# Kernel tuning notes

Measured on AMD Instinct MI355X. Metric: run time of the kernel, lower is better.

Reference implementation:

```python
import jax, jax.numpy as jnp
import numpy as np
from jax import lax

WINDOW_SIZE = 11
SIGMA = 1.5
C1 = 0.01 ** 2
C2 = 0.03 ** 2


def _gaussian_window(channel, window_size=WINDOW_SIZE, sigma=SIGMA, dtype=jnp.float32):
    x = jnp.arange(window_size, dtype=dtype) - window_size // 2
    g = jnp.exp(-(x ** 2) / (2.0 * sigma ** 2))
    g = g / g.sum()
    w2 = jnp.outer(g, g)  # [K, K]
    # depthwise kernel: [C_out=C, C_in/groups=1, K, K]
    return jnp.broadcast_to(w2[None, None], (channel, 1, window_size, window_size))


def _dwconv(x, window, channel, window_size=WINDOW_SIZE):
    pad = window_size // 2
    return lax.conv_general_dilated(
        x, window,
        window_strides=(1, 1),
        padding=[(pad, pad), (pad, pad)],
        dimension_numbers=('NCHW', 'OIHW', 'NCHW'),
        feature_group_count=channel,
    )


def setup_inputs() -> dict:
    key = jax.random.key(0)
    k1, k2 = jax.random.split(key)
    img1 = jax.random.uniform(k1, (16, 3, 512, 512), dtype=jnp.float32)
    img2 = jax.random.uniform(k2, (16, 3, 512, 512), dtype=jnp.float32)
    return {"img1": img1, "img2": img2}


def reference(img1, img2):
    channel = img1.shape[1]
    window = _gaussian_window(channel, dtype=img1.dtype)

    mu1 = _dwconv(img1, window, channel)
    mu2 = _dwconv(img2, window, channel)
    mu1_sq = mu1 * mu1
    mu2_sq = mu2 * mu2
    mu1_mu2 = mu1 * mu2

    sigma1_sq = _dwconv(img1 * img1, window, channel) - mu1_sq
    sigma2_sq = _dwconv(img2 * img2, window, channel) - mu2_sq
    sigma12 = _dwconv(img1 * img2, window, channel) - mu1_mu2

    ssim_map = ((2.0 * mu1_mu2 + C1) * (2.0 * sigma12 + C2)) / (
        (mu1_sq + mu2_sq + C1) * (sigma1_sq + sigma2_sq + C2))
    return ssim_map.mean()
```

## Files before the change

### kernel.cpp

```cpp
#include <hip/hip_runtime.h>

namespace {
constexpr int IMG_W = 512, IMG_H = 512;
constexpr int TW = 32, TH = 32;
constexpr int IN_H = TH + 10;
constexpr float C1c = 0.01f * 0.01f;
constexpr float C2c = 0.03f * 0.03f;

constexpr float GW[11] = {
    1.0283799e-03f, 7.5987582e-03f, 3.6000773e-02f, 1.0936069e-01f,
    2.1300554e-01f, 2.6601172e-01f, 2.1300554e-01f, 1.0936069e-01f,
    3.6000773e-02f, 7.5987582e-03f, 1.0283799e-03f
};

using v2f = __attribute__((ext_vector_type(2))) float;
using v4f = __attribute__((ext_vector_type(4))) float;

__device__ __forceinline__ void pkfma(v2f& acc, v2f w, v2f a) {
    asm("v_pk_fma_f32 %0, %1, %2, %0" : "+v"(acc) : "s"(w), "v"(a));
}
__device__ __forceinline__ v2f pkfma3(v2f a, v2f b, v2f c) {
    v2f d;
    asm("v_pk_fma_f32 %0, %1, %2, %3" : "=v"(d) : "v"(a), "v"(b), "v"(c));
    return d;
}
__device__ __forceinline__ v2f pkmul(v2f a, v2f b) {
    v2f d;
    asm("v_pk_mul_f32 %0, %1, %2" : "=v"(d) : "v"(a), "v"(b));
    return d;
}
__device__ __forceinline__ v2f pkadd(v2f a, v2f b) {
    v2f d;
    asm("v_pk_add_f32 %0, %1, %2" : "=v"(d) : "v"(a), "v"(b));
    return d;
}
__device__ __forceinline__ v2f bcast(float w) { v2f r; r.x = w; r.y = w; return r; }

__device__ __forceinline__ int hswz(int row, int pc) {
    return row * 16 + ((pc + row) & 15);
}
}

__global__ __launch_bounds__(256, 6) void ssim_tile_kernel(
        const float* __restrict__ img1, const float* __restrict__ img2,
        double* __restrict__ acc)
{
    union SharedU {
        v4f raw[IN_H * 23];
        struct {
            v4f hA[IN_H * 16];
            v4f hB[IN_H * 16];
        } h;
    };
    __shared__ SharedU u;
    __shared__ float wred[4];

    const int tid = threadIdx.x;
    const size_t base = (size_t)blockIdx.z * (IMG_W * IMG_H);
    const float* p1 = img1 + base;
    const float* p2 = img2 + base;
    const int x0e = blockIdx.x * TW - 6;
    const int y0  = blockIdx.y * TH - 5;

    {
        v4f* s12v4 = u.raw;
        int r   = tid / 22;
        int cf2 = tid - r * 22;
        int goff = (y0 + r) * IMG_W + x0e + 2 * cf2;
        int soff = r * 23 + cf2;
        const bool interior =
            blockIdx.x > 0 && blockIdx.x < gridDim.x - 1 &&
            blockIdx.y > 0 && blockIdx.y < gridDim.y - 1;
        if (interior) {
#pragma unroll
            for (int i = 0; i < 4; ++i) {
                if (i < 3 || tid < 924 - 3 * 256) {
                    const float2 a = *(const float2*)&p1[goff];
                    const float2 b = *(const float2*)&p2[goff];
                    v4f q; q.x = a.x; q.y = b.x; q.z = a.y; q.w = b.y;
                    s12v4[soff] = q;
                }
                const bool wrap = cf2 + 14 >= 22;
                cf2  += wrap ? -8 : 14;
                r    += wrap ? 12 : 11;
                goff += wrap ? 12 * IMG_W - 16 : 11 * IMG_W + 28;
                soff += wrap ? 12 * 23 - 8     : 11 * 23 + 14;
            }
        } else {
#pragma unroll
            for (int i = 0; i < 4; ++i) {
                if (i < 3 || tid < 924 - 3 * 256) {
                    const int gy = y0 + r;
                    const int gx = x0e + 2 * cf2;
                    float a0 = 0.f, a1 = 0.f, b0 = 0.f, b1 = 0.f;
                    if (gy >= 0 && gy < IMG_H) {
                        if (gx >= 0 && gx < IMG_W)         { a0 = p1[goff];     b0 = p2[goff]; }
                        if (gx + 1 >= 0 && gx + 1 < IMG_W) { a1 = p1[goff + 1]; b1 = p2[goff + 1]; }
                    }
                    v4f q; q.x = a0; q.y = b0; q.z = a1; q.w = b1;
                    s12v4[soff] = q;
                }
                const bool wrap = cf2 + 14 >= 22;
                cf2  += wrap ? -8 : 14;
                r    += wrap ? 12 : 11;
                goff += wrap ? 12 * IMG_W - 16 : 11 * IMG_W + 28;
                soff += wrap ? 12 * 23 - 8     : 11 * 23 + 14;
            }
        }
    }
    __syncthreads();

    v2f mu8[8], sx8[8];
    const int rA = tid >> 2;
    const int gA = tid & 3;
    const bool act2 = tid < 168;
    if (act2) {
#pragma unroll
        for (int j = 0; j < 8; ++j) { mu8[j] = bcast(0.f); sx8[j] = bcast(0.f); }
        const v4f* srow = u.raw + (rA * 23 + gA * 4);
#pragma unroll
        for (int m = 0; m < 10; ++m) {
            const v4f q = srow[m];
            const v2f* qh = (const v2f*)&q;
#pragma unroll
            for (int half = 0; half < 2; ++half) {
                const int k = 2 * m + half;
                const v2f v = qh[half];
                const v2f a2 = pkmul(v, v);
                v2f sx;
                sx.x = a2.x + a2.y;
                sx.y = v.x * v.y;
#pragma unroll
                for (int j = 0; j < 8; ++j) {
                    const int t = k - j - 1;
                    if (t >= 0 && t < 11) {
                        const v2f w2 = bcast(GW[t]);
                        pkfma(mu8[j], w2, v);
                        pkfma(sx8[j], w2, sx);
                    }
                }
            }
        }
    }
    __syncthreads();
    if (act2) {
#pragma unroll
        for (int jp = 0; jp < 4; ++jp) {
            const int j0 = 2 * jp, j1 = 2 * jp + 1;
            v4f A; A.x = mu8[j0].x; A.y = mu8[j1].x; A.z = mu8[j0].y; A.w = mu8[j1].y;
            v4f B; B.x = sx8[j0].x; B.y = sx8[j1].x; B.z = sx8[j0].y; B.w = sx8[j1].y;
            const int e = hswz(rA, 4 * gA + jp);
            u.h.hA[e] = A;
            u.h.hB[e] = B;
        }
    }
    __syncthreads();

    float lsum = 0.f;
    if (tid < 128) {
        const int pc = tid & 15;
        const int rb = (tid >> 4) * 4;
        v2f m1[4], m2[4], ssA[4], xyA[4];
#pragma unroll
        for (int j = 0; j < 4; ++j) {
            m1[j] = bcast(0.f); m2[j] = bcast(0.f);
            ssA[j] = bcast(0.f); xyA[j] = bcast(0.f);
        }
#pragma unroll
        for (int k = 0; k < 14; ++k) {
            const int e = hswz(rb + k, pc);
            const v4f A = u.h.hA[e];
            const v4f B = u.h.hB[e];
            const v2f* ah = (const v2f*)&A;
            const v2f* bh = (const v2f*)&B;
#pragma unroll
            for (int j = 0; j < 4; ++j) {
                const int t = k - j;
                if (t >= 0 && t < 11) {
                    const v2f w2 = bcast(GW[t]);
                    pkfma(m1[j],  w2, ah[0]);
                    pkfma(m2[j],  w2, ah[1]);
                    pkfma(ssA[j], w2, bh[0]);
                    pkfma(xyA[j], w2, bh[1]);
                }
            }
        }
        const v2f two  = bcast(2.f);
        const v2f c1p  = bcast(C1c);
        const v2f c2p  = bcast(C2c);
        const v2f neg1 = bcast(-1.f);
#pragma unroll
        for (int j = 0; j < 4; ++j) {
            const v2f mu12 = pkmul(m1[j], m2[j]);
            const v2f sden = pkadd(pkmul(m1[j], m1[j]), pkmul(m2[j], m2[j]));
            const v2f s12  = pkfma3(mu12, neg1, xyA[j]);
            const v2f ssum = pkfma3(sden, neg1, ssA[j]);
            const v2f num  = pkmul(pkfma3(mu12, two, c1p), pkfma3(s12, two, c2p));
            const v2f den  = pkmul(pkadd(sden, c1p), pkadd(ssum, c2p));
            lsum += __fdividef(num.x, den.x) + __fdividef(num.y, den.y);
        }
    }

#pragma unroll
    for (int off = 32; off > 0; off >>= 1)
        lsum += __shfl_down(lsum, off, 64);
    if ((tid & 63) == 0) wred[tid >> 6] = lsum;
    __syncthreads();
    if (tid == 0) {
        const int bid = (blockIdx.z * gridDim.y + blockIdx.y) * gridDim.x + blockIdx.x;
        unsafeAtomicAdd(&acc[bid & 255],
                        (double)(wred[0] + wred[1] + wred[2] + wred[3]));
    }
}

__global__ __launch_bounds__(256) void ssim_final_kernel(
        const double* __restrict__ acc, float* __restrict__ out, double inv_total)
{
    const int tid = threadIdx.x;
    double a = acc[tid];
#pragma unroll
    for (int off = 32; off > 0; off >>= 1)
        a += __shfl_down(a, off, 64);
    __shared__ double ws[4];
    if ((tid & 63) == 0) ws[tid >> 6] = a;
    __syncthreads();
    if (tid == 0)
        out[0] = (float)((ws[0] + ws[1] + ws[2] + ws[3]) * inv_total);
}

extern "C" void kernel_launch(void* const* d_in, const int* in_sizes, int n_in,
                              void* d_out, int out_size, void* d_ws, size_t ws_size,
                              hipStream_t stream)
{
    const float* img1 = (const float*)d_in[0];
    const float* img2 = (const float*)d_in[1];
    double* acc = (double*)d_ws;

    hipMemsetAsync(d_ws, 0, 256 * sizeof(double), stream);

    const int nch = in_sizes[0] / (IMG_W * IMG_H);
    dim3 grid(IMG_W / TW, IMG_H / TH, nch);
    ssim_tile_kernel<<<grid, 256, 0, stream>>>(img1, img2, acc);

    const double inv_total = 1.0 / (double)in_sizes[0];
    ssim_final_kernel<<<1, 256, 0, stream>>>(acc, (float*)d_out, inv_total);
}
```

Baseline: 152.5 us.

## Load horizontal-pass inputs directly from global memory, skipping shared staging

The horizontal convolution threads now read their 20-wide row segments straight from global memory into registers instead of first staging the input tile in shared memory. This removes the cooperative staging store, one shared read pass and two barriers, and the union aliasing of shared buffers. In exchange, overlapping halo columns are fetched redundantly from global memory (served by cache), only 168 of 256 threads issue loads, and register pressure rises from the 40 staged floats per thread.

```diff
diff --git a/kernel.cpp b/kernel.cpp
--- a/kernel.cpp
+++ b/kernel.cpp
@@ -45,14 +45,8 @@
         const float* __restrict__ img1, const float* __restrict__ img2,
         double* __restrict__ acc)
 {
-    union SharedU {
-        v4f raw[IN_H * 23];
-        struct {
-            v4f hA[IN_H * 16];
-            v4f hB[IN_H * 16];
-        } h;
-    };
-    __shared__ SharedU u;
+    __shared__ v4f hA[IN_H * 16];
+    __shared__ v4f hB[IN_H * 16];
     __shared__ float wred[4];
 
     const int tid = threadIdx.x;
@@ -62,70 +56,53 @@
     const int x0e = blockIdx.x * TW - 6;
     const int y0  = blockIdx.y * TH - 5;
 
-    {
-        v4f* s12v4 = u.raw;
-        int r   = tid / 22;
-        int cf2 = tid - r * 22;
-        int goff = (y0 + r) * IMG_W + x0e + 2 * cf2;
-        int soff = r * 23 + cf2;
+    const int rA = tid >> 2;
+    const int gA = tid & 3;
+    const bool act2 = tid < 168;
+    v2f mu8[8], sx8[8];
+    if (act2) {
+#pragma unroll
+        for (int j = 0; j < 8; ++j) { mu8[j] = bcast(0.f); sx8[j] = bcast(0.f); }
+
+        const int gy  = y0 + rA;
+        const int gxb = x0e + 8 * gA;
+        float2 u1[10], u2[10];
         const bool interior =
             blockIdx.x > 0 && blockIdx.x < gridDim.x - 1 &&
             blockIdx.y > 0 && blockIdx.y < gridDim.y - 1;
         if (interior) {
-#pragma unroll
-            for (int i = 0; i < 4; ++i) {
-                if (i < 3 || tid < 924 - 3 * 256) {
-                    const float2 a = *(const float2*)&p1[goff];
-                    const float2 b = *(const float2*)&p2[goff];
-                    v4f q; q.x = a.x; q.y = b.x; q.z = a.y; q.w = b.y;
-                    s12v4[soff] = q;
+            const float* r1 = p1 + gy * IMG_W + gxb;
+            const float* r2 = p2 + gy * IMG_W + gxb;
+#pragma unroll
+            for (int m = 0; m < 10; ++m) {
+                u1[m] = *(const float2*)(r1 + 2 * m);
+                u2[m] = *(const float2*)(r2 + 2 * m);
+            }
+        } else {
+            const bool yok = (gy >= 0) && (gy < IMG_H);
+            const float* r1 = p1 + gy * IMG_W;
+            const float* r2 = p2 + gy * IMG_W;
+#pragma unroll
+            for (int m = 0; m < 10; ++m) {
+                float a0 = 0.f, a1 = 0.f, b0 = 0.f, b1 = 0.f;
+                const int gx = gxb + 2 * m;
+                if (yok) {
+                    if (gx >= 0 && gx < IMG_W)         { a0 = r1[gx];     b0 = r2[gx]; }
+                    if (gx + 1 >= 0 && gx + 1 < IMG_W) { a1 = r1[gx + 1]; b1 = r2[gx + 1]; }
                 }
-                const bool wrap = cf2 + 14 >= 22;
-                cf2  += wrap ? -8 : 14;
-                r    += wrap ? 12 : 11;
-                goff += wrap ? 12 * IMG_W - 16 : 11 * IMG_W + 28;
-                soff += wrap ? 12 * 23 - 8     : 11 * 23 + 14;
-            }
-        } else {
-#pragma unroll
-            for (int i = 0; i < 4; ++i) {
-                if (i < 3 || tid < 924 - 3 * 256) {
-                    const int gy = y0 + r;
-                    const int gx = x0e + 2 * cf2;
-                    float a0 = 0.f, a1 = 0.f, b0 = 0.f, b1 = 0.f;
-                    if (gy >= 0 && gy < IMG_H) {
-                        if (gx >= 0 && gx < IMG_W)         { a0 = p1[goff];     b0 = p2[goff]; }
-                        if (gx + 1 >= 0 && gx + 1 < IMG_W) { a1 = p1[goff + 1]; b1 = p2[goff + 1]; }
-                    }
-                    v4f q; q.x = a0; q.y = b0; q.z = a1; q.w = b1;
-                    s12v4[soff] = q;
-                }
-                const bool wrap = cf2 + 14 >= 22;
-                cf2  += wrap ? -8 : 14;
-                r    += wrap ? 12 : 11;
-                goff += wrap ? 12 * IMG_W - 16 : 11 * IMG_W + 28;
-                soff += wrap ? 12 * 23 - 8     : 11 * 23 + 14;
-            }
-        }
-    }
-    __syncthreads();
-
-    v2f mu8[8], sx8[8];
-    const int rA = tid >> 2;
-    const int gA = tid & 3;
-    const bool act2 = tid < 168;
-    if (act2) {
-#pragma unroll
-        for (int j = 0; j < 8; ++j) { mu8[j] = bcast(0.f); sx8[j] = bcast(0.f); }
-        const v4f* srow = u.raw + (rA * 23 + gA * 4);
+                u1[m].x = a0; u1[m].y = a1;
+                u2[m].x = b0; u2[m].y = b1;
+            }
+        }
+
 #pragma unroll
         for (int m = 0; m < 10; ++m) {
-            const v4f q = srow[m];
-            const v2f* qh = (const v2f*)&q;
 #pragma unroll
             for (int half = 0; half < 2; ++half) {
                 const int k = 2 * m + half;
-                const v2f v = qh[half];
+                v2f v;
+                v.x = half ? u1[m].y : u1[m].x;
+                v.y = half ? u2[m].y : u2[m].x;
                 const v2f a2 = pkmul(v, v);
                 v2f sx;
                 sx.x = a2.x + a2.y;
@@ -141,17 +118,14 @@
                 }
             }
         }
-    }
-    __syncthreads();
-    if (act2) {
 #pragma unroll
         for (int jp = 0; jp < 4; ++jp) {
             const int j0 = 2 * jp, j1 = 2 * jp + 1;
             v4f A; A.x = mu8[j0].x; A.y = mu8[j1].x; A.z = mu8[j0].y; A.w = mu8[j1].y;
             v4f B; B.x = sx8[j0].x; B.y = sx8[j1].x; B.z = sx8[j0].y; B.w = sx8[j1].y;
             const int e = hswz(rA, 4 * gA + jp);
-            u.h.hA[e] = A;
-            u.h.hB[e] = B;
+            hA[e] = A;
+            hB[e] = B;
         }
     }
     __syncthreads();
@@ -169,8 +143,8 @@
 #pragma unroll
         for (int k = 0; k < 14; ++k) {
             const int e = hswz(rb + k, pc);
-            const v4f A = u.h.hA[e];
-            const v4f B = u.h.hB[e];
+            const v4f A = hA[e];
+            const v4f B = hB[e];
             const v2f* ah = (const v2f*)&A;
             const v2f* bh = (const v2f*)&B;
 #pragma unroll
```

After: 218.7 us. 43.4% more time.
